# Kernel tuning notes

Measured on AMD Instinct MI355X. Metric: run time of the kernel, lower is better.

The kernel has to match this reference:

```python
import jax, jax.numpy as jnp
import numpy as np

# Grid constants from voxel_size=(0.2,0.2,4), point_cloud_range=(0,-40,-3,70.4,40,1)
VX, VY, VZ = 0.2, 0.2, 4.0
PCR = (0.0, -40.0, -3.0, 70.4, 40.0, 1.0)
NX, NY, NZ = 352, 400, 1   # round((hi-lo)/v) per axis
BATCH = 2
N_POINTS = 400000
CANVAS = BATCH * NZ * NY * NX  # dense canvas of all voxels (segment ids)
EPS = 1e-3  # BN1d eps from norm_cfg


def _vidx(coors):
    # linear voxel index: b*Z*Y*X + z*Y*X + y*X + x  (coors = [b,z,y,x])
    c = coors.astype(jnp.int32)
    return ((c[:, 0] * NZ + c[:, 1]) * NY + c[:, 2]) * NX + c[:, 3]


def _seg_mean(x, idx):
    # scatter-mean over voxels (DynamicScatter, average_points=True)
    s = jax.ops.segment_sum(x, idx, num_segments=CANVAS)
    c = jax.ops.segment_sum(jnp.ones((x.shape[0], 1), x.dtype), idx, num_segments=CANVAS)
    return s / jnp.maximum(c, 1.0)


def _seg_max(x, idx):
    # scatter-max over voxels (DynamicScatter, average_points=False); empty voxels -> 0
    m = jax.ops.segment_max(x, idx, num_segments=CANVAS)
    c = jax.ops.segment_sum(jnp.ones((x.shape[0],), x.dtype), idx, num_segments=CANVAS)
    return jnp.where((c > 0)[:, None], m, jnp.zeros_like(m))


def _bn_relu(x, g, b):
    # BN1d in training mode (batch stats, biased var), affine, then ReLU
    mu = x.mean(axis=0)
    var = x.var(axis=0)
    return jax.nn.relu((x - mu) * jax.lax.rsqrt(var + EPS) * g + b)


def setup_inputs() -> dict:
    key = jax.random.key(0)
    ks = jax.random.split(key, 6)
    features = jax.random.normal(ks[0], (N_POINTS, 4), jnp.float32)
    # coors [b, z, y, x]; batch column sorted so coors[-1,0]+1 == batch_size
    half = N_POINTS // 2
    b = jnp.concatenate([jnp.zeros(half, jnp.int32), jnp.ones(N_POINTS - half, jnp.int32)])
    z = jnp.zeros(N_POINTS, jnp.int32)  # NZ == 1
    y = jax.random.randint(ks[1], (N_POINTS,), 0, NY, jnp.int32)
    x = jax.random.randint(ks[2], (N_POINTS,), 0, NX, jnp.int32)
    coors = jnp.stack([b, z, y, x], axis=1)
    # VFE params: layer0 Linear(10->64, no bias), layer1 Linear(128->128, no bias)
    W0 = jax.random.normal(ks[3], (10, 64), jnp.float32) * 0.1
    g0 = jnp.ones((64,), jnp.float32)
    b0 = jnp.zeros((64,), jnp.float32)
    W1 = jax.random.normal(ks[4], (128, 128), jnp.float32) * 0.1
    g1 = jnp.ones((128,), jnp.float32)
    b1 = jnp.zeros((128,), jnp.float32)
    return {"features": features, "coors": coors, "W0": W0, "g0": g0, "b0": b0,
            "W1": W1, "g1": g1, "b1": b1}


def reference(features, coors, W0, g0, b0, W1, g1, b1):
    idx = _vidx(coors)
    # cluster center: scatter-mean of point features, gather back to points
    vmean = _seg_mean(features, idx)
    pts_mean = vmean[idx]
    f_cluster = features[:, :3] - pts_mean[:, :3]
    # voxel center offset
    cf = coors.astype(features.dtype)
    f_center = jnp.stack([
        features[:, 0] - (cf[:, 3] * VX + (VX / 2 + PCR[0])),
        features[:, 1] - (cf[:, 2] * VY + (VY / 2 + PCR[1])),
        features[:, 2] - (cf[:, 1] * VZ + (VZ / 2 + PCR[2])),
    ], axis=1)
    feat = jnp.concatenate([features, f_cluster, f_center], axis=1)  # (N, 10)
    # VFE layer 0 + voxel max pool + gather-broadcast + concat
    pf0 = _bn_relu(feat @ W0, g0, b0)           # (N, 64)
    v0 = _seg_max(pf0, idx)                     # (CANVAS, 64)
    feat1 = jnp.concatenate([pf0, v0[idx]], axis=1)  # (N, 128)
    # VFE layer 1 + final voxel max pool
    pf1 = _bn_relu(feat1 @ W1, g1, b1)          # (N, 128)
    voxel_feats = _seg_max(pf1, idx)            # (CANVAS, 128), dense canvas
    return voxel_feats
```

## Files before the change

kernel.cpp:

```cpp
#include <hip/hip_runtime.h>

#define NPTS 400000
#define NXv 352
#define NYv 400
#define CANVAS 281600
#define G2B 512
#define SCANB 275

typedef unsigned int uint;
typedef unsigned short ushort;
typedef __attribute__((ext_vector_type(8))) short short8;
typedef __attribute__((ext_vector_type(4))) float floatx4;

__device__ inline uint packbf(float a, float b) {
    uint ua = __float_as_uint(a);
    ua = (ua + 0x7fffu + ((ua >> 16) & 1u)) >> 16;
    uint ub = __float_as_uint(b);
    ub = (ub + 0x7fffu + ((ub >> 16) & 1u)) & 0xffff0000u;
    return ua | ub;
}
__device__ inline ushort bf16bits(float a) {
    uint u = __float_as_uint(a);
    return (ushort)((u + 0x7fffu + ((u >> 16) & 1u)) >> 16);
}
__device__ inline float lo16(uint u) { return __uint_as_float(u << 16); }
__device__ inline float hi16(uint u) { return __uint_as_float(u & 0xffff0000u); }
__device__ inline float bfval(ushort u) { return __uint_as_float(((uint)u) << 16); }

__global__ void k_bucket(const int4* __restrict__ coors, const float* __restrict__ W1,
                         int* __restrict__ idxbuf, int* __restrict__ pidx,
                         uint* __restrict__ ucnt, ushort* __restrict__ w1t) {
    int b = blockIdx.x;
    if (b < 1563) {
        int i = b * 256 + threadIdx.x;
        if (i >= NPTS) return;
        int4 c = coors[i];
        int idx = ((c.x + c.y) * NYv + c.z) * NXv + c.w;
        idxbuf[i] = idx;
        pidx[i] = (int)atomicAdd(&ucnt[idx], 1u);
    } else {
        int i = (b - 1563) * 256 + threadIdx.x;
        int n = i & 127, k = i >> 7;
        w1t[n * 128 + k] = bf16bits(W1[k * 128 + n]);
    }
}

__global__ __launch_bounds__(1024) void k_scanA(const uint* __restrict__ ucnt,
                                                uint* __restrict__ voff,
                                                uint* __restrict__ bsum) {
    __shared__ uint sh[1024];
    int t = threadIdx.x;
    int v = blockIdx.x * 1024 + t;
    uint val = ucnt[v];
    sh[t] = val;
    for (int off = 1; off < 1024; off <<= 1) {
        __syncthreads();
        uint x = (t >= off) ? sh[t - off] : 0u;
        __syncthreads();
        sh[t] += x;
    }
    uint incl = sh[t];
    voff[v] = incl - val;
    if (t == 1023) bsum[blockIdx.x] = incl;
}

__global__ __launch_bounds__(1024) void k_scanC(const uint* __restrict__ bsum,
                                                uint* __restrict__ voff) {
    __shared__ uint sh[1024];
    __shared__ uint bs[1024];
    int t = threadIdx.x;
    uint val = (t < SCANB) ? bsum[t] : 0u;
    sh[t] = val; bs[t] = val;
    for (int off = 1; off < 1024; off <<= 1) {
        __syncthreads();
        uint x = (t >= off) ? sh[t - off] : 0u;
        __syncthreads();
        sh[t] += x;
    }
    __syncthreads();
    uint off_ = sh[blockIdx.x] - bs[blockIdx.x];
    int v = blockIdx.x * 1024 + t;
    voff[v] += off_;
    if (blockIdx.x == SCANB - 1 && t == 1023) voff[CANVAS] = NPTS;
}

__global__ void k_perm(const int* __restrict__ idxbuf, const int* __restrict__ pidx,
                       const uint* __restrict__ voff, const float4* __restrict__ feat,
                       int* __restrict__ vidx, float4* __restrict__ featS) {
    int i = blockIdx.x * 256 + threadIdx.x;
    if (i >= NPTS) return;
    int idx = idxbuf[i];
    uint j = voff[idx] + (uint)pidx[i];
    vidx[j] = idx;
    featS[j] = feat[i];
}

__global__ void k_vmean(const float4* __restrict__ featS, const uint* __restrict__ voff,
                        float4* __restrict__ vmean) {
    int v = blockIdx.x * 256 + threadIdx.x;
    if (v >= CANVAS) return;
    uint s_ = voff[v], e_ = voff[v + 1];
    float4 s = make_float4(0.f, 0.f, 0.f, 0.f);
    for (uint j = s_; j < e_; ++j) {
        float4 f = featS[j];
        s.x += f.x; s.y += f.y; s.z += f.z; s.w += f.w;
    }
    float inv = 1.0f / (float)max((int)(e_ - s_), 1);
    vmean[v] = make_float4(s.x * inv, s.y * inv, s.z * inv, s.w * inv);
}

__global__ __launch_bounds__(256) void k_gemm1(
        const float4* __restrict__ featS, const int* __restrict__ vidx,
        const float4* __restrict__ vmean, const float* __restrict__ W0,
        uint* __restrict__ x0u, float* __restrict__ stats) {
    __shared__ float w0s[640];
    __shared__ __align__(8) ushort tile[256 * 68];
    __shared__ float ps[128], qs[128];
    for (int t = threadIdx.x; t < 640; t += 256) w0s[t] = W0[t];
    __syncthreads();
    int j = blockIdx.x * 256 + threadIdx.x;
    bool valid = j < NPTS;
    ushort* trow = &tile[threadIdx.x * 68];
    if (valid) {
        float4 f = featS[j];
        int idx = vidx[j];
        float4 vm = vmean[idx];
        int xq = idx % NXv;
        int yq = (idx / NXv) % NYv;
        float ft[10];
        ft[0] = f.x; ft[1] = f.y; ft[2] = f.z; ft[3] = f.w;
        ft[4] = f.x - vm.x;
        ft[5] = f.y - vm.y;
        ft[6] = f.z - vm.z;
        ft[7] = f.x - ((float)xq * 0.2f + 0.1f);
        ft[8] = f.y - ((float)yq * 0.2f - 39.9f);
        ft[9] = f.z + 1.0f;
        uint* o = x0u + (size_t)j * 32;
        #pragma unroll
        for (int g = 0; g < 8; ++g) {
            float a[8];
            #pragma unroll
            for (int q = 0; q < 8; ++q) a[q] = 0.f;
            #pragma unroll
            for (int k = 0; k < 10; ++k) {
                float fk = ft[k];
                #pragma unroll
                for (int q = 0; q < 8; ++q) a[q] = fmaf(fk, w0s[k * 64 + g * 8 + q], a[q]);
            }
            uint4 w;
            w.x = packbf(a[0], a[1]); w.y = packbf(a[2], a[3]);
            w.z = packbf(a[4], a[5]); w.w = packbf(a[6], a[7]);
            *(uint4*)(o + g * 4) = w;
            ((uint2*)trow)[g * 2 + 0] = make_uint2(w.x, w.y);
            ((uint2*)trow)[g * 2 + 1] = make_uint2(w.z, w.w);
        }
    } else {
        #pragma unroll
        for (int g = 0; g < 16; ++g) ((uint2*)trow)[g] = make_uint2(0u, 0u);
    }
    __syncthreads();
    if (threadIdx.x < 128) {
        int c = threadIdx.x & 63, half = threadIdx.x >> 6;
        float s = 0.f, q = 0.f;
        for (int r = half * 128; r < half * 128 + 128; ++r) {
            float xv = bfval(tile[r * 68 + c]);
            s += xv;
            q = fmaf(xv, xv, q);
        }
        ps[half * 64 + c] = s;
        qs[half * 64 + c] = q;
    }
    __syncthreads();
    if (threadIdx.x < 64) {
        int c = threadIdx.x;
        atomicAdd(&stats[c], ps[c] + ps[64 + c]);
        atomicAdd(&stats[64 + c], qs[c] + qs[64 + c]);
    }
}

__global__ void k_vmax0(const uint* __restrict__ x0u, const uint* __restrict__ voff,
                        const float* __restrict__ stats, const float* __restrict__ g0,
                        const float* __restrict__ b0, uint* __restrict__ v0u) {
    __shared__ float s[128];
    if (threadIdx.x < 64) {
        int c = threadIdx.x;
        float mu = stats[c] * (1.0f / NPTS);
        float var = stats[64 + c] * (1.0f / NPTS) - mu * mu;
        float sc = (1.0f / sqrtf(var + 1e-3f)) * g0[c];
        s[c] = sc;
        s[64 + c] = fmaf(-mu, sc, b0[c]);
    }
    __syncthreads();
    int t = blockIdx.x * 256 + threadIdx.x;
    int v = t >> 4;
    if (v >= CANVAS) return;
    uint s_ = voff[v], e_ = voff[v + 1];
    if (s_ == e_) return;
    int c = (t & 15) << 2;
    float4 m = make_float4(0.f, 0.f, 0.f, 0.f);
    for (uint j = s_; j < e_; ++j) {
        uint2 u = *(const uint2*)(x0u + (size_t)j * 32 + (c >> 1));
        m.x = fmaxf(m.x, fmaf(lo16(u.x), s[c + 0], s[64 + c + 0]));
        m.y = fmaxf(m.y, fmaf(hi16(u.x), s[c + 1], s[64 + c + 1]));
        m.z = fmaxf(m.z, fmaf(lo16(u.y), s[c + 2], s[64 + c + 2]));
        m.w = fmaxf(m.w, fmaf(hi16(u.y), s[c + 3], s[64 + c + 3]));
    }
    uint2 o; o.x = packbf(m.x, m.y); o.y = packbf(m.z, m.w);
    *(uint2*)(v0u + (size_t)v * 32 + (c >> 1)) = o;
}

__global__ __launch_bounds__(256) void k_gemm2p(
        const uint* __restrict__ x0u, const uint* __restrict__ v0u,
        const int* __restrict__ vidx, const uint* __restrict__ voff,
        const float* __restrict__ stats, const float* __restrict__ g0,
        const float* __restrict__ b0, const ushort* __restrict__ w1t,
        ushort* __restrict__ vmaxc, float* __restrict__ sums) {
    __shared__ __align__(16) ushort As[64 * 136];
    __shared__ __align__(8) ushort CsT[128 * 74];
    __shared__ float s[128];
    __shared__ int svid[2][64];

    int lane = threadIdx.x & 63, wid = threadIdx.x >> 6;
    int m = lane & 15, q = lane >> 4;

    if (threadIdx.x < 64) {
        int c = threadIdx.x;
        float mu = stats[c] * (1.0f / NPTS);
        float var = stats[64 + c] * (1.0f / NPTS) - mu * mu;
        float sc = (1.0f / sqrtf(var + 1e-3f)) * g0[c];
        s[c] = sc;
        s[64 + c] = fmaf(-mu, sc, b0[c]);
    }

    short8 breg[8][4];
    #pragma unroll
    for (int ct = 0; ct < 8; ++ct) {
        const ushort* br = &w1t[(ct * 16 + m) * 128 + q * 8];
        #pragma unroll
        for (int ks = 0; ks < 4; ++ks)
            breg[ct][ks] = *(const short8*)&br[ks * 32];
    }

    int p0 = (int)((long long)blockIdx.x * NPTS / G2B);
    int p1 = (int)((long long)(blockIdx.x + 1) * NPTS / G2B);
    int ps, pe;
    { int v = vidx[p0]; ps = (voff[v] == (uint)p0) ? p0 : (int)voff[v + 1]; }
    if (p1 >= NPTS) pe = NPTS;
    else { int v = vidx[p1]; pe = (voff[v] == (uint)p1) ? p1 : (int)voff[v + 1]; }

    float run = -3.0e38f, csum = 0.f, csq = 0.f;
    int vcur = -1;

    auto stage = [&](int r0s, int p) {
        int nrows = min(64, pe - r0s);
        for (int i = threadIdx.x; i < 512; i += 128) {
            int r = i >> 3, ch = i & 7, cb = ch * 8;
            uint4 o4 = make_uint4(0u, 0u, 0u, 0u);
            if (r < nrows) {
                uint4 u = *(const uint4*)(x0u + (size_t)(r0s + r) * 32 + ch * 4);
                uint w[4] = {u.x, u.y, u.z, u.w}, o[4];
                #pragma unroll
                for (int q2 = 0; q2 < 4; ++q2) {
                    float a = fmaxf(fmaf(lo16(w[q2]), s[cb + 2 * q2], s[64 + cb + 2 * q2]), 0.f);
                    float b = fmaxf(fmaf(hi16(w[q2]), s[cb + 2 * q2 + 1], s[64 + cb + 2 * q2 + 1]), 0.f);
                    o[q2] = packbf(a, b);
                }
                o4 = make_uint4(o[0], o[1], o[2], o[3]);
            }
            *(uint4*)&As[r * 136 + ch * 8] = o4;
        }
        for (int i = threadIdx.x; i < 512; i += 128) {
            int r = i >> 3, ch = i & 7;
            uint4 u = make_uint4(0u, 0u, 0u, 0u);
            if (r < nrows) u = *(const uint4*)(v0u + (size_t)vidx[r0s + r] * 32 + ch * 4);
            *(uint4*)&As[r * 136 + 64 + ch * 8] = u;
        }
        if (threadIdx.x < 64)
            svid[p][threadIdx.x] = (threadIdx.x < nrows) ? vidx[r0s + threadIdx.x] : -1;
    };

    __syncthreads();
    if (threadIdx.x < 128 && ps < pe) stage(ps, 0);
    __syncthreads();

    int sp = 0;
    for (int r0 = ps; r0 < pe; r0 += 64, sp ^= 1) {
        const ushort* ar = &As[(wid * 16 + m) * 136 + q * 8];
        short8 a0 = *(const short8*)&ar[0];
        short8 a1 = *(const short8*)&ar[32];
        short8 a2 = *(const short8*)&ar[64];
        short8 a3 = *(const short8*)&ar[96];
        #pragma unroll
        for (int ct = 0; ct < 8; ++ct) {
            floatx4 acc = {0.f, 0.f, 0.f, 0.f};
            acc = __builtin_amdgcn_mfma_f32_16x16x32_bf16(a0, breg[ct][0], acc, 0, 0, 0);
            acc = __builtin_amdgcn_mfma_f32_16x16x32_bf16(a1, breg[ct][1], acc, 0, 0, 0);
            acc = __builtin_amdgcn_mfma_f32_16x16x32_bf16(a2, breg[ct][2], acc, 0, 0, 0);
            acc = __builtin_amdgcn_mfma_f32_16x16x32_bf16(a3, breg[ct][3], acc, 0, 0, 0);
            uint* cp = (uint*)&CsT[(ct * 16 + m) * 74 + wid * 16 + q * 4];
            cp[0] = packbf(acc[0], acc[1]);
            cp[1] = packbf(acc[2], acc[3]);
        }
        __syncthreads();

        if (threadIdx.x < 128) {
            if (r0 + 64 < pe) stage(r0 + 64, sp ^ 1);
        } else {
            int c = threadIdx.x - 128;
            const uint* crow = (const uint*)&CsT[c * 74];
            #pragma unroll 4
            for (int rp = 0; rp < 32; ++rp) {
                uint u = crow[rp];
                int va = svid[sp][2 * rp], vb = svid[sp][2 * rp + 1];
                float xa = lo16(u), xb = hi16(u);
                bool brk = (va != vcur);
                if (brk && vcur >= 0) vmaxc[(size_t)vcur * 128 + c] = bf16bits(run);
                run = brk ? xa : fmaxf(run, xa);
                vcur = va;
                csum += xa; csq = fmaf(xa, xa, csq);
                brk = (vb != vcur);
                if (brk && vcur >= 0) vmaxc[(size_t)vcur * 128 + c] = bf16bits(run);
                run = brk ? xb : fmaxf(run, xb);
                vcur = vb;
                csum += xb; csq = fmaf(xb, xb, csq);
            }
        }
        __syncthreads();
    }

    if (threadIdx.x >= 128) {
        int c = threadIdx.x - 128;
        if (vcur >= 0) vmaxc[(size_t)vcur * 128 + c] = bf16bits(run);
        atomicAdd(&sums[c], csum);
        atomicAdd(&sums[128 + c], csq);
    }
}

__global__ __launch_bounds__(256) void k_bnout(const ushort* __restrict__ vmaxc,
        const uint* __restrict__ voff, const float* __restrict__ stats,
        const float* __restrict__ g1, const float* __restrict__ b1,
        float4* __restrict__ out) {
    __shared__ float s[256];
    if (threadIdx.x < 128) {
        int c = threadIdx.x;
        float mu = stats[128 + c] * (1.0f / NPTS);
        float var = stats[256 + c] * (1.0f / NPTS) - mu * mu;
        float sc = (1.0f / sqrtf(var + 1e-3f)) * g1[c];
        s[c] = sc;
        s[128 + c] = fmaf(-mu, sc, b1[c]);
    }
    __syncthreads();
    int t = blockIdx.x * 256 + threadIdx.x;
    int v = t >> 5;
    if (v >= CANVAS) return;
    int c = (t & 31) << 2;
    float4 m = make_float4(0.f, 0.f, 0.f, 0.f);
    if (voff[v + 1] != voff[v]) {
        uint2 u = *(const uint2*)(vmaxc + (size_t)v * 128 + c);
        m.x = fmaxf(fmaf(lo16(u.x), s[c + 0], s[128 + c + 0]), 0.f);
        m.y = fmaxf(fmaf(hi16(u.x), s[c + 1], s[128 + c + 1]), 0.f);
        m.z = fmaxf(fmaf(lo16(u.y), s[c + 2], s[128 + c + 2]), 0.f);
        m.w = fmaxf(fmaf(hi16(u.y), s[c + 3], s[128 + c + 3]), 0.f);
    }
    out[(size_t)v * 32 + (c >> 2)] = m;
}

extern "C" void kernel_launch(void* const* d_in, const int* in_sizes, int n_in,
                              void* d_out, int out_size, void* d_ws, size_t ws_size,
                              hipStream_t stream) {
    const float4* feat  = (const float4*)d_in[0];
    const int4*   coors = (const int4*)d_in[1];
    const float*  W0    = (const float*)d_in[2];
    const float*  g0    = (const float*)d_in[3];
    const float*  b0    = (const float*)d_in[4];
    const float*  W1    = (const float*)d_in[5];
    const float*  g1    = (const float*)d_in[6];
    const float*  b1    = (const float*)d_in[7];

    char* ws = (char*)d_ws;
    int*    idxbuf = (int*)(ws + 0);
    int*    pidx   = (int*)(ws + 1600000);
    uint*   ucnt   = (uint*)(ws + 3200000);
    float*  stats  = (float*)(ws + 4326400);
    uint*   voff   = (uint*)(ws + 4329472);
    uint*   bsum   = (uint*)(ws + 5455888);
    int*    vidx   = (int*)(ws + 5459984);
    float*  featS  = (float*)(ws + 7059984);
    float*  vmean  = (float*)(ws + 13459984);
    ushort* w1t    = (ushort*)(ws + 17965584);
    uint*   x0u    = (uint*)(ws + 17998352);
    uint*   v0u    = (uint*)(ws + 69198352);
    ushort* vmaxc  = (ushort*)(ws + 105243152);

    hipMemsetAsync(ws + 3200000, 0, 1129472, stream);

    const int BLK = 256;
    int gpts = (NPTS + BLK - 1) / BLK;
    int gvox = (CANVAS + BLK - 1) / BLK;

    k_bucket<<<gpts + 64, BLK, 0, stream>>>(coors, W1, idxbuf, pidx, ucnt, w1t);
    k_scanA<<<SCANB, 1024, 0, stream>>>(ucnt, voff, bsum);
    k_scanC<<<SCANB, 1024, 0, stream>>>(bsum, voff);
    k_perm<<<gpts, BLK, 0, stream>>>(idxbuf, pidx, voff, feat, vidx, (float4*)featS);
    k_vmean<<<gvox, BLK, 0, stream>>>((const float4*)featS, voff, (float4*)vmean);
    k_gemm1<<<gpts, BLK, 0, stream>>>((const float4*)featS, vidx, (const float4*)vmean,
                                      W0, x0u, stats);
    k_vmax0<<<CANVAS * 16 / BLK, BLK, 0, stream>>>(x0u, voff, stats, g0, b0, v0u);
    k_gemm2p<<<G2B, BLK, 0, stream>>>(x0u, v0u, vidx, voff, stats, g0, b0, w1t,
                                      vmaxc, stats + 128);
    k_bnout<<<CANVAS * 32 / BLK, BLK, 0, stream>>>(vmaxc, voff, stats, g1, b1,
                                                   (float4*)d_out);
}
```

Measured before the change: 441.9 us.

## Precompute BN0+ReLU activations in vmax0 and stage GEMM2 tiles via global_load_lds

k_vmax0 now applies the layer-0 BN+ReLU once per point and writes the normalized bf16 activations to a new buffer x0b, while also taking the voxel max over the ReLU'd values. k_gemm2p drops its own BN recompute and, for full 64-row tiles, copies x0b rows and gathered v0 rows straight into a double-buffered, unpadded LDS tile with global_load_lds DMA. Voxel ids for the next tile are prefetched during the MFMA phase. The cost is an extra 51 MB write and read of x0b, and the unpadded LDS layout may add bank conflicts on the A-fragment reads.

```diff
diff --git a/kernel.cpp b/kernel.cpp
--- a/kernel.cpp
+++ b/kernel.cpp
@@ -26,6 +26,12 @@
 __device__ inline float lo16(uint u) { return __uint_as_float(u << 16); }
 __device__ inline float hi16(uint u) { return __uint_as_float(u & 0xffff0000u); }
 __device__ inline float bfval(ushort u) { return __uint_as_float(((uint)u) << 16); }
+
+__device__ inline void gload_lds16(const uint* g, ushort* l) {
+    __builtin_amdgcn_global_load_lds((const __attribute__((address_space(1))) void*)g,
+                                     (__attribute__((address_space(3))) void*)l,
+                                     16, 0, 0);
+}
 
 __global__ void k_bucket(const int4* __restrict__ coors, const float* __restrict__ W1,
                          int* __restrict__ idxbuf, int* __restrict__ pidx,
@@ -180,7 +186,8 @@
 
 __global__ void k_vmax0(const uint* __restrict__ x0u, const uint* __restrict__ voff,
                         const float* __restrict__ stats, const float* __restrict__ g0,
-                        const float* __restrict__ b0, uint* __restrict__ v0u) {
+                        const float* __restrict__ b0, uint* __restrict__ v0u,
+                        uint* __restrict__ x0b) {
     __shared__ float s[128];
     if (threadIdx.x < 64) {
         int c = threadIdx.x;
@@ -200,37 +207,30 @@
     float4 m = make_float4(0.f, 0.f, 0.f, 0.f);
     for (uint j = s_; j < e_; ++j) {
         uint2 u = *(const uint2*)(x0u + (size_t)j * 32 + (c >> 1));
-        m.x = fmaxf(m.x, fmaf(lo16(u.x), s[c + 0], s[64 + c + 0]));
-        m.y = fmaxf(m.y, fmaf(hi16(u.x), s[c + 1], s[64 + c + 1]));
-        m.z = fmaxf(m.z, fmaf(lo16(u.y), s[c + 2], s[64 + c + 2]));
-        m.w = fmaxf(m.w, fmaf(hi16(u.y), s[c + 3], s[64 + c + 3]));
+        float a = fmaxf(fmaf(lo16(u.x), s[c + 0], s[64 + c + 0]), 0.f);
+        float b = fmaxf(fmaf(hi16(u.x), s[c + 1], s[64 + c + 1]), 0.f);
+        float cc = fmaxf(fmaf(lo16(u.y), s[c + 2], s[64 + c + 2]), 0.f);
+        float d = fmaxf(fmaf(hi16(u.y), s[c + 3], s[64 + c + 3]), 0.f);
+        m.x = fmaxf(m.x, a); m.y = fmaxf(m.y, b);
+        m.z = fmaxf(m.z, cc); m.w = fmaxf(m.w, d);
+        uint2 o2; o2.x = packbf(a, b); o2.y = packbf(cc, d);
+        *(uint2*)(x0b + (size_t)j * 32 + (c >> 1)) = o2;
     }
     uint2 o; o.x = packbf(m.x, m.y); o.y = packbf(m.z, m.w);
     *(uint2*)(v0u + (size_t)v * 32 + (c >> 1)) = o;
 }
 
 __global__ __launch_bounds__(256) void k_gemm2p(
-        const uint* __restrict__ x0u, const uint* __restrict__ v0u,
+        const uint* __restrict__ x0b, const uint* __restrict__ v0u,
         const int* __restrict__ vidx, const uint* __restrict__ voff,
-        const float* __restrict__ stats, const float* __restrict__ g0,
-        const float* __restrict__ b0, const ushort* __restrict__ w1t,
+        const ushort* __restrict__ w1t,
         ushort* __restrict__ vmaxc, float* __restrict__ sums) {
-    __shared__ __align__(16) ushort As[64 * 136];
+    __shared__ __align__(16) ushort As[2 * 64 * 128];
     __shared__ __align__(8) ushort CsT[128 * 74];
-    __shared__ float s[128];
     __shared__ int svid[2][64];
 
     int lane = threadIdx.x & 63, wid = threadIdx.x >> 6;
     int m = lane & 15, q = lane >> 4;
-
-    if (threadIdx.x < 64) {
-        int c = threadIdx.x;
-        float mu = stats[c] * (1.0f / NPTS);
-        float var = stats[64 + c] * (1.0f / NPTS) - mu * mu;
-        float sc = (1.0f / sqrtf(var + 1e-3f)) * g0[c];
-        s[c] = sc;
-        s[64 + c] = fmaf(-mu, sc, b0[c]);
-    }
 
     short8 breg[8][4];
     #pragma unroll
@@ -251,45 +251,55 @@
     float run = -3.0e38f, csum = 0.f, csq = 0.f;
     int vcur = -1;
 
-    auto stage = [&](int r0s, int p) {
+    auto stageM = [&](int r0s, int bufn) {
         int nrows = min(64, pe - r0s);
-        for (int i = threadIdx.x; i < 512; i += 128) {
-            int r = i >> 3, ch = i & 7, cb = ch * 8;
-            uint4 o4 = make_uint4(0u, 0u, 0u, 0u);
+        for (int i = threadIdx.x; i < 1024; i += 128) {
+            int r = i >> 4, ch = i & 15;
+            uint4 u = make_uint4(0u, 0u, 0u, 0u);
             if (r < nrows) {
-                uint4 u = *(const uint4*)(x0u + (size_t)(r0s + r) * 32 + ch * 4);
-                uint w[4] = {u.x, u.y, u.z, u.w}, o[4];
-                #pragma unroll
-                for (int q2 = 0; q2 < 4; ++q2) {
-                    float a = fmaxf(fmaf(lo16(w[q2]), s[cb + 2 * q2], s[64 + cb + 2 * q2]), 0.f);
-                    float b = fmaxf(fmaf(hi16(w[q2]), s[cb + 2 * q2 + 1], s[64 + cb + 2 * q2 + 1]), 0.f);
-                    o[q2] = packbf(a, b);
-                }
-                o4 = make_uint4(o[0], o[1], o[2], o[3]);
+                const uint* srcp = (ch < 8)
+                    ? (x0b + (size_t)(r0s + r) * 32 + ch * 4)
+                    : (v0u + (size_t)vidx[r0s + r] * 32 + (ch - 8) * 4);
+                u = *(const uint4*)srcp;
             }
-            *(uint4*)&As[r * 136 + ch * 8] = o4;
-        }
-        for (int i = threadIdx.x; i < 512; i += 128) {
-            int r = i >> 3, ch = i & 7;
-            uint4 u = make_uint4(0u, 0u, 0u, 0u);
-            if (r < nrows) u = *(const uint4*)(v0u + (size_t)vidx[r0s + r] * 32 + ch * 4);
-            *(uint4*)&As[r * 136 + 64 + ch * 8] = u;
-        }
-        if (threadIdx.x < 64)
-            svid[p][threadIdx.x] = (threadIdx.x < nrows) ? vidx[r0s + threadIdx.x] : -1;
+            *(uint4*)&As[bufn * 8192 + r * 128 + ch * 8] = u;
+        }
     };
-
-    __syncthreads();
-    if (threadIdx.x < 128 && ps < pe) stage(ps, 0);
+    auto stageDMA = [&](int r0n, int bufn) {
+        int j0 = wid * 8;
+        #pragma unroll
+        for (int j = j0; j < j0 + 8; ++j) {
+            int rl = j * 4 + (lane >> 4);
+            int p = lane & 15;
+            int vr = svid[bufn][rl];
+            const uint* s32 = (p < 8)
+                ? (x0b + (size_t)(r0n + rl) * 32 + p * 4)
+                : (v0u + (size_t)vr * 32 + (p - 8) * 4);
+            gload_lds16(s32, &As[bufn * 8192 + j * 512]);
+        }
+    };
+
+    if (threadIdx.x < 64) {
+        int nr0 = (ps < pe) ? min(64, pe - ps) : 0;
+        svid[0][threadIdx.x] = (threadIdx.x < nr0) ? vidx[ps + threadIdx.x] : -1;
+    }
+    if (threadIdx.x < 128 && ps < pe) stageM(ps, 0);
     __syncthreads();
 
     int sp = 0;
     for (int r0 = ps; r0 < pe; r0 += 64, sp ^= 1) {
-        const ushort* ar = &As[(wid * 16 + m) * 136 + q * 8];
-        short8 a0 = *(const short8*)&ar[0];
-        short8 a1 = *(const short8*)&ar[32];
-        short8 a2 = *(const short8*)&ar[64];
-        short8 a3 = *(const short8*)&ar[96];
+        int spn = sp ^ 1;
+        bool hasnext = (r0 + 64 < pe);
+        int vn = -1;
+        if (hasnext && threadIdx.x < 64) {
+            int rn = r0 + 64 + threadIdx.x;
+            if (rn < pe) vn = vidx[rn];
+        }
+        const ushort* ab = &As[sp * 8192 + (wid * 16 + m) * 128 + q * 8];
+        short8 a0 = *(const short8*)&ab[0];
+        short8 a1 = *(const short8*)&ab[32];
+        short8 a2 = *(const short8*)&ab[64];
+        short8 a3 = *(const short8*)&ab[96];
         #pragma unroll
         for (int ct = 0; ct < 8; ++ct) {
             floatx4 acc = {0.f, 0.f, 0.f, 0.f};
@@ -301,10 +311,15 @@
             cp[0] = packbf(acc[0], acc[1]);
             cp[1] = packbf(acc[2], acc[3]);
         }
+        if (hasnext && threadIdx.x < 64) svid[spn][threadIdx.x] = vn;
         __syncthreads();
 
         if (threadIdx.x < 128) {
-            if (r0 + 64 < pe) stage(r0 + 64, sp ^ 1);
+            if (hasnext) {
+                if (r0 + 128 <= pe) stageDMA(r0 + 64, spn);
+                else stageM(r0 + 64, spn);
+            }
+            asm volatile("s_waitcnt vmcnt(0)" ::: "memory");
         } else {
             int c = threadIdx.x - 128;
             const uint* crow = (const uint*)&CsT[c * 74];
@@ -391,6 +406,7 @@
     uint*   x0u    = (uint*)(ws + 17998352);
     uint*   v0u    = (uint*)(ws + 69198352);
     ushort* vmaxc  = (ushort*)(ws + 105243152);
+    uint*   x0b    = (uint*)(ws + 177332752);
 
     hipMemsetAsync(ws + 3200000, 0, 1129472, stream);
 
@@ -405,9 +421,8 @@
     k_vmean<<<gvox, BLK, 0, stream>>>((const float4*)featS, voff, (float4*)vmean);
     k_gemm1<<<gpts, BLK, 0, stream>>>((const float4*)featS, vidx, (const float4*)vmean,
                                       W0, x0u, stats);
-    k_vmax0<<<CANVAS * 16 / BLK, BLK, 0, stream>>>(x0u, voff, stats, g0, b0, v0u);
-    k_gemm2p<<<G2B, BLK, 0, stream>>>(x0u, v0u, vidx, voff, stats, g0, b0, w1t,
-                                      vmaxc, stats + 128);
+    k_vmax0<<<CANVAS * 16 / BLK, BLK, 0, stream>>>(x0u, voff, stats, g0, b0, v0u, x0b);
+    k_gemm2p<<<G2B, BLK, 0, stream>>>(x0b, v0u, vidx, voff, w1t, vmaxc, stats + 128);
     k_bnout<<<CANVAS * 32 / BLK, BLK, 0, stream>>>(vmaxc, voff, stats, g1, b1,
                                                    (float4*)d_out);
 }
```

Result: slower. 452.5 us (+2.4%).
